# Optimization experiments

Hardware: AMD Instinct MI355X
Metric: run time of the kernel (lower is better)

## Reference

```python
import jax, jax.numpy as jnp
import numpy as np


def conv1x1(x, w, b):
    # x: [B, Cin, D, H, W], w: [Cout, Cin], b: [Cout]
    return jnp.einsum('bcdhw,oc->bodhw', x, w) + b[None, :, None, None, None]


def setup_inputs() -> dict:
    key = jax.random.key(0)
    ks = jax.random.split(key, 9)
    B, C, D, H, W = 2, 64, 16, 16, 16
    Cc = 64          # context_dim
    C8 = C // 8      # inner attention dim
    s = 0.05
    return {
        'x': jax.random.normal(ks[0], (B, C, D, H, W), jnp.float32),
        'context': jax.random.normal(ks[1], (B, Cc, D, H, W), jnp.float32),
        'Wq': jax.random.normal(ks[2], (C8, C), jnp.float32) * s,
        'bq': jax.random.normal(ks[3], (C8,), jnp.float32) * s,
        'Wk': jax.random.normal(ks[4], (C8, Cc), jnp.float32) * s,
        'bk': jax.random.normal(ks[5], (C8,), jnp.float32) * s,
        'Wv': jax.random.normal(ks[6], (C, Cc), jnp.float32) * s,
        'bv': jax.random.normal(ks[7], (C,), jnp.float32) * s,
        'gamma': jax.random.normal(ks[8], (1,), jnp.float32) * s,
    }


def reference(x, context, Wq, bq, Wk, bk, Wv, bv, gamma):
    B, C, D, H, W = x.shape
    N = D * H * W
    q = conv1x1(x, Wq, bq).reshape(B, -1, N)        # [B, C/8, N]
    k = conv1x1(context, Wk, bk).reshape(B, -1, N)  # [B, C/8, N]
    v = conv1x1(context, Wv, bv).reshape(B, C, N)   # [B, C, N]
    # energy[b, n, m] = q[:, :, n] . k[:, :, m]  (no scaling, as in source)
    energy = jnp.einsum('bcn,bcm->bnm', q, k)       # [B, N, N]
    attn = jax.nn.softmax(energy, axis=-1)
    # out = v @ attn^T : out[b, c, n] = sum_m v[b, c, m] * attn[b, n, m]
    out = jnp.einsum('bcm,bnm->bcn', v, attn).reshape(B, C, D, H, W)
    return gamma[0] * out + x
```

## Files before the change

### kernel.cpp

```cpp
#include <hip/hip_runtime.h>

#define NTOK 4096

typedef __attribute__((ext_vector_type(8))) short short8;
typedef __attribute__((ext_vector_type(4))) float f32x4;

__device__ __forceinline__ unsigned short f2bf(float f) {
    unsigned u = __float_as_uint(f);
    u += 0x7fffu + ((u >> 16) & 1u);
    return (unsigned short)(u >> 16);
}

__global__ __launch_bounds__(256) void proj(
    const float* __restrict__ x, const float* __restrict__ ctx,
    const float* __restrict__ Wq, const float* __restrict__ bq,
    const float* __restrict__ Wk, const float* __restrict__ bk,
    const float* __restrict__ Wv, const float* __restrict__ bv,
    unsigned short* __restrict__ qbf, unsigned short* __restrict__ kbf,
    unsigned short* __restrict__ vtp)
{
    __shared__ float sW[16 * 64];
    __shared__ float sB[16];
    int tid  = threadIdx.x;
    int ogrp = blockIdx.z;
    int b    = blockIdx.y;
    int n0   = blockIdx.x * 64;

    if (ogrp == 0) {
        for (int i = tid; i < 1024; i += 256)
            sW[i] = (i < 512) ? Wq[i] : Wk[i - 512];
        if (tid < 16) sB[tid] = (tid < 8) ? bq[tid] : bk[tid - 8];
    } else {
        for (int i = tid; i < 1024; i += 256)
            sW[i] = Wv[(ogrp - 1) * 1024 + i];
        if (tid < 16) sB[tid] = bv[(ogrp - 1) * 16 + tid];
    }
    __syncthreads();

    int nn   = tid & 63;
    int osub = tid >> 6;
    const float* inp = (ogrp == 0 && osub < 2) ? x : ctx;
    const float* ip  = inp + (size_t)b * 64 * NTOK + n0 + nn;

    float a0 = sB[osub * 4 + 0], a1 = sB[osub * 4 + 1];
    float a2 = sB[osub * 4 + 2], a3 = sB[osub * 4 + 3];
#pragma unroll 8
    for (int c = 0; c < 64; ++c) {
        float val = ip[(size_t)c * NTOK];
        a0 += sW[(osub * 4 + 0) * 64 + c] * val;
        a1 += sW[(osub * 4 + 1) * 64 + c] * val;
        a2 += sW[(osub * 4 + 2) * 64 + c] * val;
        a3 += sW[(osub * 4 + 3) * 64 + c] * val;
    }
    float av[4] = {a0, a1, a2, a3};

    if (ogrp == 0) {
        if (osub < 2) {
            ushort4 pk = {f2bf(av[0]), f2bf(av[1]), f2bf(av[2]), f2bf(av[3])};
            *(ushort4*)&qbf[((size_t)b * NTOK + n0 + nn) * 8 + osub * 4] = pk;
        } else {
            ushort4 pk = {f2bf(av[0]), f2bf(av[1]), f2bf(av[2]), f2bf(av[3])};
            *(ushort4*)&kbf[((size_t)b * NTOK + n0 + nn) * 8 + (osub - 2) * 4] = pk;
        }
    } else {
        int cbase = (ogrp - 1) * 16 + osub * 4;
        int m  = n0 + nn;
        int g  = m & ~31;
        int mm = m & 31;
        int p  = ((mm >> 2) & 3) * 8 + (mm >> 4) * 4 + (mm & 3);
#pragma unroll
        for (int j = 0; j < 4; ++j)
            vtp[((size_t)b * 64 + cbase + j) * NTOK + g + p] = f2bf(av[j]);
    }
}

__global__ __launch_bounds__(512, 4) void attn2(
    const unsigned short* __restrict__ qbf, const unsigned short* __restrict__ kbf,
    const unsigned short* __restrict__ vtp, const float* __restrict__ x,
    const float* __restrict__ gamma, float* __restrict__ out)
{
    __shared__ float sO[8][64][17];
    __shared__ float sL[8][16];

    int tid  = threadIdx.x;
    int w    = tid >> 6, lane = tid & 63;
    int n    = lane & 15, quad = lane >> 4;
    int b    = blockIdx.y;
    int n0   = blockIdx.x * 16;

    const f32x4 z4 = {0.f, 0.f, 0.f, 0.f};
    short8 bqf = {0, 0, 0, 0, 0, 0, 0, 0};
    if (quad == 0)
        bqf = *(const short8*)&qbf[((size_t)b * NTOK + n0 + n) * 8];

    const unsigned short* kb = kbf + (size_t)b * NTOK * 8;
    const unsigned short* vb = vtp + (size_t)b * 64 * NTOK;

    f32x4 acc[4];
#pragma unroll
    for (int ct = 0; ct < 4; ++ct) acc[ct] = z4;
    float lsum = 0.f;

    for (int mt = 0; mt < 4; ++mt) {
        int m0 = w * 512 + mt * 128;

        f32x4 sa[8];
#pragma unroll
        for (int t = 0; t < 8; ++t) {
            short8 ak = {0, 0, 0, 0, 0, 0, 0, 0};
            if (quad == 0)
                ak = *(const short8*)&kb[(size_t)(m0 + t * 16 + n) * 8];
            sa[t] = __builtin_amdgcn_mfma_f32_16x16x32_bf16(ak, bqf, z4, 0, 0, 0);
        }

#pragma unroll
        for (int s = 0; s < 4; ++s) {
            float e0 = __expf(sa[2 * s][0]), e1 = __expf(sa[2 * s][1]);
            float e2 = __expf(sa[2 * s][2]), e3 = __expf(sa[2 * s][3]);
            float e4 = __expf(sa[2 * s + 1][0]), e5 = __expf(sa[2 * s + 1][1]);
            float e6 = __expf(sa[2 * s + 1][2]), e7 = __expf(sa[2 * s + 1][3]);
            lsum += ((e0 + e1) + (e2 + e3)) + ((e4 + e5) + (e6 + e7));
            short8 pf;
            pf[0] = (short)f2bf(e0); pf[1] = (short)f2bf(e1);
            pf[2] = (short)f2bf(e2); pf[3] = (short)f2bf(e3);
            pf[4] = (short)f2bf(e4); pf[5] = (short)f2bf(e5);
            pf[6] = (short)f2bf(e6); pf[7] = (short)f2bf(e7);
#pragma unroll
            for (int ct = 0; ct < 4; ++ct) {
                short8 avf = *(const short8*)&vb[(size_t)(ct * 16 + n) * NTOK
                                                 + m0 + s * 32 + quad * 8];
                acc[ct] = __builtin_amdgcn_mfma_f32_16x16x32_bf16(avf, pf, acc[ct], 0, 0, 0);
            }
        }
    }

    lsum += __shfl_xor(lsum, 16);
    lsum += __shfl_xor(lsum, 32);
    if (lane < 16) sL[w][n] = lsum;
#pragma unroll
    for (int ct = 0; ct < 4; ++ct)
#pragma unroll
        for (int r = 0; r < 4; ++r)
            sO[w][ct * 16 + quad * 4 + r][n] = acc[ct][r];
    __syncthreads();

    int c  = tid >> 3;
    int ng = (tid & 7) * 2;
    float g = gamma[0];
    float L0 = 0.f, L1 = 0.f, v0 = 0.f, v1 = 0.f;
#pragma unroll
    for (int w2 = 0; w2 < 8; ++w2) {
        L0 += sL[w2][ng];     L1 += sL[w2][ng + 1];
        v0 += sO[w2][c][ng];  v1 += sO[w2][c][ng + 1];
    }
    size_t ob = ((size_t)b * 64 + c) * NTOK + n0 + ng;
    float2 xv = *(const float2*)&x[ob];
    float2 ov = {g * (v0 / L0) + xv.x, g * (v1 / L1) + xv.y};
    *(float2*)&out[ob] = ov;
}

extern "C" void kernel_launch(void* const* d_in, const int* in_sizes, int n_in,
                              void* d_out, int out_size, void* d_ws, size_t ws_size,
                              hipStream_t stream) {
    const float* x     = (const float*)d_in[0];
    const float* ctx   = (const float*)d_in[1];
    const float* Wq    = (const float*)d_in[2];
    const float* bq    = (const float*)d_in[3];
    const float* Wk    = (const float*)d_in[4];
    const float* bk    = (const float*)d_in[5];
    const float* Wv    = (const float*)d_in[6];
    const float* bv    = (const float*)d_in[7];
    const float* gamma = (const float*)d_in[8];
    float* out = (float*)d_out;

    unsigned short* qbf = (unsigned short*)d_ws;
    unsigned short* kbf = qbf + 2 * NTOK * 8;
    unsigned short* vtp = kbf + 2 * NTOK * 8;

    proj<<<dim3(64, 2, 5), 256, 0, stream>>>(x, ctx, Wq, bq, Wk, bk, Wv, bv, qbf, kbf, vtp);
    attn2<<<dim3(NTOK / 16, 2), 512, 0, stream>>>(qbf, kbf, vtp, x, gamma, out);
}
```

Baseline: 112.3 us.

## Pad Q/K to 32 channels, software-pipeline K/V loads, use exp2 with truncating pack

Q and K are written zero-padded to 32 bf16 per token, so every lane loads its fragment without the quad==0 branch. Q is prescaled by log2(e) so the softmax can use exp2f. The attention loop is restructured into 8 steps of 64 keys, with K and V fragments for the next step prefetched into registers while the current MFMAs and exponentials run. The exponentials are packed to bf16 with a byte-perm that truncates instead of rounding. The costs are four times the Q/K workspace and write traffic, more live registers, and slightly different rounding.

```diff
diff --git a/kernel.cpp b/kernel.cpp
--- a/kernel.cpp
+++ b/kernel.cpp
@@ -4,11 +4,16 @@
 
 typedef __attribute__((ext_vector_type(8))) short short8;
 typedef __attribute__((ext_vector_type(4))) float f32x4;
+typedef __attribute__((ext_vector_type(4))) unsigned int uint4v;
 
 __device__ __forceinline__ unsigned short f2bf(float f) {
     unsigned u = __float_as_uint(f);
     u += 0x7fffu + ((u >> 16) & 1u);
     return (unsigned short)(u >> 16);
+}
+
+__device__ __forceinline__ unsigned int pk2(float lo, float hi) {
+    return __builtin_amdgcn_perm(__float_as_uint(hi), __float_as_uint(lo), 0x07060302u);
 }
 
 __global__ __launch_bounds__(256) void proj(
@@ -16,7 +21,7 @@
     const float* __restrict__ Wq, const float* __restrict__ bq,
     const float* __restrict__ Wk, const float* __restrict__ bk,
     const float* __restrict__ Wv, const float* __restrict__ bv,
-    unsigned short* __restrict__ qbf, unsigned short* __restrict__ kbf,
+    unsigned short* __restrict__ qbf32, unsigned short* __restrict__ kbf32,
     unsigned short* __restrict__ vtp)
 {
     __shared__ float sW[16 * 64];
@@ -44,7 +49,7 @@
 
     float a0 = sB[osub * 4 + 0], a1 = sB[osub * 4 + 1];
     float a2 = sB[osub * 4 + 2], a3 = sB[osub * 4 + 3];
-#pragma unroll 8
+#pragma unroll 16
     for (int c = 0; c < 64; ++c) {
         float val = ip[(size_t)c * NTOK];
         a0 += sW[(osub * 4 + 0) * 64 + c] * val;
@@ -55,12 +60,22 @@
     float av[4] = {a0, a1, a2, a3};
 
     if (ogrp == 0) {
-        if (osub < 2) {
-            ushort4 pk = {f2bf(av[0]), f2bf(av[1]), f2bf(av[2]), f2bf(av[3])};
-            *(ushort4*)&qbf[((size_t)b * NTOK + n0 + nn) * 8 + osub * 4] = pk;
+        bool isq = osub < 2;
+        float sc = isq ? 1.4426950408889634f : 1.0f;
+        unsigned short* dst = isq ? qbf32 : kbf32;
+        int half = osub & 1;
+        size_t base = ((size_t)b * NTOK + n0 + nn) * 32;
+        ushort4 pk = {f2bf(av[0] * sc), f2bf(av[1] * sc), f2bf(av[2] * sc), f2bf(av[3] * sc)};
+        *(ushort4*)&dst[base + half * 4] = pk;
+        ushort4 z = {0, 0, 0, 0};
+        if (half == 0) {
+            *(ushort4*)&dst[base + 8]  = z;
+            *(ushort4*)&dst[base + 12] = z;
+            *(ushort4*)&dst[base + 16] = z;
         } else {
-            ushort4 pk = {f2bf(av[0]), f2bf(av[1]), f2bf(av[2]), f2bf(av[3])};
-            *(ushort4*)&kbf[((size_t)b * NTOK + n0 + nn) * 8 + (osub - 2) * 4] = pk;
+            *(ushort4*)&dst[base + 20] = z;
+            *(ushort4*)&dst[base + 24] = z;
+            *(ushort4*)&dst[base + 28] = z;
         }
     } else {
         int cbase = (ogrp - 1) * 16 + osub * 4;
@@ -74,8 +89,8 @@
     }
 }
 
-__global__ __launch_bounds__(512, 4) void attn2(
-    const unsigned short* __restrict__ qbf, const unsigned short* __restrict__ kbf,
+__global__ __launch_bounds__(512, 4) void attn3(
+    const unsigned short* __restrict__ qbf32, const unsigned short* __restrict__ kbf32,
     const unsigned short* __restrict__ vtp, const float* __restrict__ x,
     const float* __restrict__ gamma, float* __restrict__ out)
 {
@@ -89,54 +104,70 @@
     int n0   = blockIdx.x * 16;
 
     const f32x4 z4 = {0.f, 0.f, 0.f, 0.f};
-    short8 bqf = {0, 0, 0, 0, 0, 0, 0, 0};
-    if (quad == 0)
-        bqf = *(const short8*)&qbf[((size_t)b * NTOK + n0 + n) * 8];
-
-    const unsigned short* kb = kbf + (size_t)b * NTOK * 8;
-    const unsigned short* vb = vtp + (size_t)b * 64 * NTOK;
-
-    f32x4 acc[4];
-#pragma unroll
-    for (int ct = 0; ct < 4; ++ct) acc[ct] = z4;
+    short8 bq = *(const short8*)&qbf32[((size_t)b * NTOK + n0 + n) * 32 + quad * 8];
+
+    const unsigned short* kb = kbf32 + (size_t)b * NTOK * 32;
+    const unsigned short* vb = vtp   + (size_t)b * 64 * NTOK;
+    int mbase = w * 512;
+
+#define KLD(h, t) (*(const short8*)&kb[((size_t)(mbase + (h) * 64 + (t) * 16 + n)) * 32 + quad * 8])
+#define VLD(h, s, ct) (*(const short8*)&vb[(size_t)((ct) * 16 + n) * NTOK + mbase + (h) * 64 + (s) * 32 + quad * 8])
+
+    f32x4 acc0 = z4, acc1 = z4, acc2 = z4, acc3 = z4;
     float lsum = 0.f;
 
-    for (int mt = 0; mt < 4; ++mt) {
-        int m0 = w * 512 + mt * 128;
-
-        f32x4 sa[8];
-#pragma unroll
-        for (int t = 0; t < 8; ++t) {
-            short8 ak = {0, 0, 0, 0, 0, 0, 0, 0};
-            if (quad == 0)
-                ak = *(const short8*)&kb[(size_t)(m0 + t * 16 + n) * 8];
-            sa[t] = __builtin_amdgcn_mfma_f32_16x16x32_bf16(ak, bqf, z4, 0, 0, 0);
+    short8 kf0 = KLD(0, 0), kf1 = KLD(0, 1), kf2 = KLD(0, 2), kf3 = KLD(0, 3);
+    short8 af0 = VLD(0, 0, 0), af1 = VLD(0, 0, 1), af2 = VLD(0, 0, 2), af3 = VLD(0, 0, 3);
+    short8 af4 = VLD(0, 1, 0), af5 = VLD(0, 1, 1), af6 = VLD(0, 1, 2), af7 = VLD(0, 1, 3);
+
+    for (int h = 0; h < 8; ++h) {
+        f32x4 sa0 = __builtin_amdgcn_mfma_f32_16x16x32_bf16(kf0, bq, z4, 0, 0, 0);
+        f32x4 sa1 = __builtin_amdgcn_mfma_f32_16x16x32_bf16(kf1, bq, z4, 0, 0, 0);
+        f32x4 sa2 = __builtin_amdgcn_mfma_f32_16x16x32_bf16(kf2, bq, z4, 0, 0, 0);
+        f32x4 sa3 = __builtin_amdgcn_mfma_f32_16x16x32_bf16(kf3, bq, z4, 0, 0, 0);
+        if (h < 7) {
+            kf0 = KLD(h + 1, 0); kf1 = KLD(h + 1, 1);
+            kf2 = KLD(h + 1, 2); kf3 = KLD(h + 1, 3);
         }
 
-#pragma unroll
-        for (int s = 0; s < 4; ++s) {
-            float e0 = __expf(sa[2 * s][0]), e1 = __expf(sa[2 * s][1]);
-            float e2 = __expf(sa[2 * s][2]), e3 = __expf(sa[2 * s][3]);
-            float e4 = __expf(sa[2 * s + 1][0]), e5 = __expf(sa[2 * s + 1][1]);
-            float e6 = __expf(sa[2 * s + 1][2]), e7 = __expf(sa[2 * s + 1][3]);
-            lsum += ((e0 + e1) + (e2 + e3)) + ((e4 + e5) + (e6 + e7));
-            short8 pf;
-            pf[0] = (short)f2bf(e0); pf[1] = (short)f2bf(e1);
-            pf[2] = (short)f2bf(e2); pf[3] = (short)f2bf(e3);
-            pf[4] = (short)f2bf(e4); pf[5] = (short)f2bf(e5);
-            pf[6] = (short)f2bf(e6); pf[7] = (short)f2bf(e7);
-#pragma unroll
-            for (int ct = 0; ct < 4; ++ct) {
-                short8 avf = *(const short8*)&vb[(size_t)(ct * 16 + n) * NTOK
-                                                 + m0 + s * 32 + quad * 8];
-                acc[ct] = __builtin_amdgcn_mfma_f32_16x16x32_bf16(avf, pf, acc[ct], 0, 0, 0);
-            }
+        float e00 = exp2f(sa0[0]), e01 = exp2f(sa0[1]), e02 = exp2f(sa0[2]), e03 = exp2f(sa0[3]);
+        float e10 = exp2f(sa1[0]), e11 = exp2f(sa1[1]), e12 = exp2f(sa1[2]), e13 = exp2f(sa1[3]);
+        float e20 = exp2f(sa2[0]), e21 = exp2f(sa2[1]), e22 = exp2f(sa2[2]), e23 = exp2f(sa2[3]);
+        float e30 = exp2f(sa3[0]), e31 = exp2f(sa3[1]), e32 = exp2f(sa3[2]), e33 = exp2f(sa3[3]);
+        lsum += ((e00 + e01) + (e02 + e03)) + ((e10 + e11) + (e12 + e13))
+              + ((e20 + e21) + (e22 + e23)) + ((e30 + e31) + (e32 + e33));
+
+        uint4v t0, t1;
+        t0[0] = pk2(e00, e01); t0[1] = pk2(e02, e03);
+        t0[2] = pk2(e10, e11); t0[3] = pk2(e12, e13);
+        t1[0] = pk2(e20, e21); t1[1] = pk2(e22, e23);
+        t1[2] = pk2(e30, e31); t1[3] = pk2(e32, e33);
+        short8 pf0 = __builtin_bit_cast(short8, t0);
+        short8 pf1 = __builtin_bit_cast(short8, t1);
+
+        acc0 = __builtin_amdgcn_mfma_f32_16x16x32_bf16(af0, pf0, acc0, 0, 0, 0);
+        acc1 = __builtin_amdgcn_mfma_f32_16x16x32_bf16(af1, pf0, acc1, 0, 0, 0);
+        acc2 = __builtin_amdgcn_mfma_f32_16x16x32_bf16(af2, pf0, acc2, 0, 0, 0);
+        acc3 = __builtin_amdgcn_mfma_f32_16x16x32_bf16(af3, pf0, acc3, 0, 0, 0);
+        acc0 = __builtin_amdgcn_mfma_f32_16x16x32_bf16(af4, pf1, acc0, 0, 0, 0);
+        acc1 = __builtin_amdgcn_mfma_f32_16x16x32_bf16(af5, pf1, acc1, 0, 0, 0);
+        acc2 = __builtin_amdgcn_mfma_f32_16x16x32_bf16(af6, pf1, acc2, 0, 0, 0);
+        acc3 = __builtin_amdgcn_mfma_f32_16x16x32_bf16(af7, pf1, acc3, 0, 0, 0);
+
+        if (h < 7) {
+            af0 = VLD(h + 1, 0, 0); af1 = VLD(h + 1, 0, 1);
+            af2 = VLD(h + 1, 0, 2); af3 = VLD(h + 1, 0, 3);
+            af4 = VLD(h + 1, 1, 0); af5 = VLD(h + 1, 1, 1);
+            af6 = VLD(h + 1, 1, 2); af7 = VLD(h + 1, 1, 3);
         }
     }
+#undef KLD
+#undef VLD
 
     lsum += __shfl_xor(lsum, 16);
     lsum += __shfl_xor(lsum, 32);
     if (lane < 16) sL[w][n] = lsum;
+    f32x4 acc[4] = {acc0, acc1, acc2, acc3};
 #pragma unroll
     for (int ct = 0; ct < 4; ++ct)
 #pragma unroll
@@ -173,10 +204,10 @@
     const float* gamma = (const float*)d_in[8];
     float* out = (float*)d_out;
 
-    unsigned short* qbf = (unsigned short*)d_ws;
-    unsigned short* kbf = qbf + 2 * NTOK * 8;
-    unsigned short* vtp = kbf + 2 * NTOK * 8;
-
-    proj<<<dim3(64, 2, 5), 256, 0, stream>>>(x, ctx, Wq, bq, Wk, bk, Wv, bv, qbf, kbf, vtp);
-    attn2<<<dim3(NTOK / 16, 2), 512, 0, stream>>>(qbf, kbf, vtp, x, gamma, out);
-}
+    unsigned short* qbf32 = (unsigned short*)d_ws;
+    unsigned short* kbf32 = qbf32 + 2 * NTOK * 32;
+    unsigned short* vtp   = kbf32 + 2 * NTOK * 32;
+
+    proj<<<dim3(64, 2, 5), 256, 0, stream>>>(x, ctx, Wq, bq, Wk, bk, Wv, bv, qbf32, kbf32, vtp);
+    attn3<<<dim3(NTOK / 16, 2), 512, 0, stream>>>(qbf32, kbf32, vtp, x, gamma, out);
+}
```

New measurement: 114.6 us. No clear change (+2.0%).
